# Kernel tuning notes

Measured on AMD Instinct MI355X. Metric: run time of the kernel, lower is better.

Reference implementation:

```python
import jax, jax.numpy as jnp
import numpy as np

B, T, D_IN, H, NH, R = 32, 1024, 64, 128, 4, 3
HD = H // NH  # 32


def _p(key, shape, scale=0.02):
    return jax.random.normal(key, shape, dtype=jnp.float32) * scale


def setup_inputs() -> dict:
    key = jax.random.key(0)
    ks = jax.random.split(key, 8)
    return {
        "x": jax.random.normal(ks[0], (B, T, D_IN), dtype=jnp.float32),
        "theta_w": _p(ks[1], (H, D_IN)),
        "theta_b": jnp.zeros((H,), jnp.float32),
        "in_proj_w": _p(ks[2], (3 * H, H)),
        "in_proj_b": jnp.zeros((3 * H,), jnp.float32),
        "out_proj_w": _p(ks[3], (H, H)),
        "out_proj_b": jnp.zeros((H,), jnp.float32),
        "ln_g": jnp.ones((H,), jnp.float32),
        "ln_b": jnp.zeros((H,), jnp.float32),
        "w1": _p(ks[4], (H, H)),
        "b1": jnp.zeros((H,), jnp.float32),
        "w2": _p(ks[5], (2, H)),
        "b2": jnp.zeros((2,), jnp.float32),
    }


def _build_adj(t, radius):
    # banded adjacency: adj[i,j] = 1/(1+|i-j|) for |i-j| <= radius, row-normalized
    idx = jnp.arange(t)
    d = jnp.abs(idx[:, None] - idx[None, :])
    adj = jnp.where(d <= radius, 1.0 / (1.0 + d.astype(jnp.float32)), 0.0)
    return adj / jnp.clip(adj.sum(axis=1, keepdims=True), 1e-8)


def reference(x, theta_w, theta_b, in_proj_w, in_proj_b, out_proj_w, out_proj_b,
              ln_g, ln_b, w1, b1, w2, b2):
    h = x @ theta_w.T + theta_b                       # [B,T,H]
    adj = _build_adj(T, R)                            # [T,T]
    g = jnp.einsum('ij,bjh->bih', adj, h)             # banded temporal aggregation

    # torch nn.MultiheadAttention (batch_first, eval -> no dropout)
    qkv = g @ in_proj_w.T + in_proj_b                 # [B,T,3H]
    q, k, v = jnp.split(qkv, 3, axis=-1)
    split_heads = lambda t: t.reshape(B, T, NH, HD).transpose(0, 2, 1, 3)
    q, k, v = split_heads(q), split_heads(k), split_heads(v)
    scores = jnp.einsum('bntd,bnsd->bnts', q, k) / jnp.sqrt(jnp.float32(HD))
    attn = jax.nn.softmax(scores, axis=-1)
    o = jnp.einsum('bnts,bnsd->bntd', attn, v)
    o = o.transpose(0, 2, 1, 3).reshape(B, T, H)
    a = o @ out_proj_w.T + out_proj_b                 # [B,T,H]

    # head on last timestep: LayerNorm -> Linear -> GELU(exact) -> Linear
    last = a[:, -1, :]                                # [B,H]
    mu = last.mean(-1, keepdims=True)
    var = ((last - mu) ** 2).mean(-1, keepdims=True)
    ln = (last - mu) / jnp.sqrt(var + 1e-5) * ln_g + ln_b
    hid = jax.nn.gelu(ln @ w1.T + b1, approximate=False)
    return hid @ w2.T + b2                            # [B,2]
```

## Files before the change

### kernel.cpp

```cpp
#include <hip/hip_runtime.h>
#include <math.h>

#define TT 1024

__global__ __launch_bounds__(256) void k_combine(
    const float* __restrict__ theta_w, const float* __restrict__ theta_b,
    const float* __restrict__ ipw, const float* __restrict__ ipb,
    float* __restrict__ C, float* __restrict__ bqv) {
  __shared__ float s_ipw[128 * 129];
  __shared__ float s_tw2[2][128];
  const int bidx = blockIdx.x;
  const int tid = threadIdx.x;
  if (bidx < 96) {
    const int m = bidx >> 5;
    const int dpair = bidx & 31;
    const float4* g4 = (const float4*)(ipw + m * 128 * 128);
    for (int it = 0; it < 16; ++it) {
      int idx4 = tid + it * 256;
      float4 v = g4[idx4];
      int idx = idx4 * 4;
      int e = idx >> 7;
      int c = idx & 127;
      float* dst = &s_ipw[e * 129 + c];
      dst[0] = v.x; dst[1] = v.y; dst[2] = v.z; dst[3] = v.w;
    }
    {
      int dd = tid >> 7, cc = tid & 127;
      s_tw2[dd][cc] = theta_w[cc * 64 + dpair * 2 + dd];
    }
    __syncthreads();
    const int dd = tid >> 7;
    const int e = tid & 127;
    const float* row = &s_ipw[e * 129];
    const float* tw = s_tw2[dd];
    float acc = 0.f;
    for (int c = 0; c < 128; ++c) acc += tw[c] * row[c];
    C[m * 8192 + (dpair * 2 + dd) * 128 + e] = acc;
  } else {
    const int e = tid & 127;
    const int which = tid >> 7;
    const int r0 = which ? (256 + e) : e;
    const float* row = ipw + r0 * 128;
    float acc = ipb[r0];
    for (int c = 0; c < 128; ++c) acc += theta_b[c] * row[c];
    bqv[which * 128 + e] = acc;
  }
}

__global__ __launch_bounds__(256) void k_attn(
    const float* __restrict__ x, const float* __restrict__ C,
    const float* __restrict__ bqv, float* __restrict__ o_out) {
  const int b = blockIdx.x >> 2;
  const int n = blockIdx.x & 3;
  const int tid = threadIdx.x;
  __shared__ float s_xs[64];
  __shared__ float s_q[32];
  __shared__ __align__(16) float s_r[64];
  __shared__ float s_t[TT];
  __shared__ float s_p[TT];
  __shared__ float s_pt[TT];
  __shared__ float s_red[4];
  __shared__ __align__(16) float s_uacc[4][64];
  __shared__ float s_u[64];

  const float* __restrict__ xb = x + (size_t)b * TT * 64;
  const float* Cq = C;
  const float* Ck = C + 8192;
  const float* Cv = C + 16384;

  if (tid < 64) {
    float acc = xb[(TT - 1) * 64 + tid]
              + 0.5f        * xb[(TT - 2) * 64 + tid]
              + (1.f / 3.f) * xb[(TT - 3) * 64 + tid]
              + 0.25f       * xb[(TT - 4) * 64 + tid];
    s_xs[tid] = acc * (12.f / 25.f);
  }
  __syncthreads();
  if (tid < 32) {
    float acc = bqv[n * 32 + tid];
    for (int d = 0; d < 64; ++d) acc += Cq[d * 128 + n * 32 + tid] * s_xs[d];
    s_q[tid] = acc;
  }
  __syncthreads();
  if (tid < 64) {
    float acc = 0.f;
    const float* ckr = Ck + tid * 128 + n * 32;
    for (int e = 0; e < 32; ++e) acc += ckr[e] * s_q[e];
    s_r[tid] = acc * 0.17677669529663687f;
  }
  __syncthreads();

  const int g = tid >> 4;
  const int l = tid & 15;
  const float4 r4 = ((const float4*)s_r)[l];
  for (int it = 0; it < 64; ++it) {
    const int j = it * 16 + g;
    const float4 xv = ((const float4*)(xb + j * 64))[l];
    float part = xv.x * r4.x + xv.y * r4.y + xv.z * r4.z + xv.w * r4.w;
    part += __shfl_xor(part, 1);
    part += __shfl_xor(part, 2);
    part += __shfl_xor(part, 4);
    part += __shfl_xor(part, 8);
    if (l == 0) s_t[j] = part;
  }
  __syncthreads();

  float sc[4], wsv[4];
  float lmax = -1e30f;
  const int s0 = tid * 4;
  for (int k = 0; k < 4; ++k) {
    const int s = s0 + k;
    float acc = 0.f, wsum = 0.f;
    #pragma unroll
    for (int dj = -3; dj <= 3; ++dj) {
      const int j = s + dj;
      if (j >= 0 && j < TT) {
        const float w = 1.f / (1.f + (float)(dj < 0 ? -dj : dj));
        acc += w * s_t[j];
        wsum += w;
      }
    }
    sc[k] = acc / wsum;
    wsv[k] = wsum;
    lmax = fmaxf(lmax, sc[k]);
  }
  #pragma unroll
  for (int m = 32; m >= 1; m >>= 1) lmax = fmaxf(lmax, __shfl_xor(lmax, m));
  if ((tid & 63) == 0) s_red[tid >> 6] = lmax;
  __syncthreads();
  const float bmax = fmaxf(fmaxf(s_red[0], s_red[1]), fmaxf(s_red[2], s_red[3]));
  __syncthreads();
  float lsum = 0.f;
  for (int k = 0; k < 4; ++k) {
    const float e = expf(sc[k] - bmax);
    lsum += e;
    s_p[s0 + k] = e / wsv[k];
  }
  #pragma unroll
  for (int m = 32; m >= 1; m >>= 1) lsum += __shfl_xor(lsum, m);
  if ((tid & 63) == 0) s_red[tid >> 6] = lsum;
  __syncthreads();
  const float denom = s_red[0] + s_red[1] + s_red[2] + s_red[3];
  const float inv_denom = 1.f / denom;

  for (int k = 0; k < 4; ++k) {
    const int j = s0 + k;
    float acc = 0.f;
    #pragma unroll
    for (int dj = -3; dj <= 3; ++dj) {
      const int s = j + dj;
      if (s >= 0 && s < TT)
        acc += (1.f / (1.f + (float)(dj < 0 ? -dj : dj))) * s_p[s];
    }
    s_pt[j] = acc;
  }
  __syncthreads();

  float4 u4 = make_float4(0.f, 0.f, 0.f, 0.f);
  for (int it = 0; it < 64; ++it) {
    const int j = it * 16 + g;
    const float pj = s_pt[j];
    const float4 xv = ((const float4*)(xb + j * 64))[l];
    u4.x += pj * xv.x; u4.y += pj * xv.y; u4.z += pj * xv.z; u4.w += pj * xv.w;
  }
  u4.x += __shfl_xor(u4.x, 16); u4.y += __shfl_xor(u4.y, 16);
  u4.z += __shfl_xor(u4.z, 16); u4.w += __shfl_xor(u4.w, 16);
  u4.x += __shfl_xor(u4.x, 32); u4.y += __shfl_xor(u4.y, 32);
  u4.z += __shfl_xor(u4.z, 32); u4.w += __shfl_xor(u4.w, 32);
  const int wv = tid >> 6;
  if ((tid & 63) < 16) ((float4*)s_uacc[wv])[tid & 15] = u4;
  __syncthreads();
  if (tid < 64) {
    s_u[tid] = (s_uacc[0][tid] + s_uacc[1][tid] + s_uacc[2][tid] + s_uacc[3][tid]) * inv_denom;
  }
  __syncthreads();
  if (tid < 32) {
    float acc = bqv[128 + n * 32 + tid];
    for (int d = 0; d < 64; ++d) acc += Cv[d * 128 + n * 32 + tid] * s_u[d];
    o_out[b * 128 + n * 32 + tid] = acc;
  }
}

__global__ __launch_bounds__(128) void k_epilogue(
    const float* __restrict__ o, const float* __restrict__ Wout,
    const float* __restrict__ outb, const float* __restrict__ ln_g,
    const float* __restrict__ ln_b, const float* __restrict__ w1,
    const float* __restrict__ b1, const float* __restrict__ w2,
    const float* __restrict__ b2, float* __restrict__ out) {
  const int b = blockIdx.x;
  const int e = threadIdx.x;
  __shared__ float s_o[128], s_ln[128], s_hid[128], s_red[2];
  s_o[e] = o[b * 128 + e];
  __syncthreads();
  float a = outb[e];
  {
    const float* wr = Wout + e * 128;
    for (int f = 0; f < 128; ++f) a += wr[f] * s_o[f];
  }
  float sum = a;
  #pragma unroll
  for (int m = 32; m >= 1; m >>= 1) sum += __shfl_xor(sum, m);
  if ((e & 63) == 0) s_red[e >> 6] = sum;
  __syncthreads();
  const float mu = (s_red[0] + s_red[1]) * (1.f / 128.f);
  __syncthreads();
  const float d = a - mu;
  float sq = d * d;
  #pragma unroll
  for (int m = 32; m >= 1; m >>= 1) sq += __shfl_xor(sq, m);
  if ((e & 63) == 0) s_red[e >> 6] = sq;
  __syncthreads();
  const float var = (s_red[0] + s_red[1]) * (1.f / 128.f);
  const float ln = d / sqrtf(var + 1e-5f) * ln_g[e] + ln_b[e];
  s_ln[e] = ln;
  __syncthreads();
  float h = b1[e];
  {
    const float* w1r = w1 + e * 128;
    for (int f = 0; f < 128; ++f) h += w1r[f] * s_ln[f];
  }
  h = 0.5f * h * (1.f + erff(h * 0.70710678118654752f));
  s_hid[e] = h;
  __syncthreads();
  if (e < 2) {
    float acc = b2[e];
    const float* w2r = w2 + e * 128;
    for (int f = 0; f < 128; ++f) acc += w2r[f] * s_hid[f];
    out[b * 2 + e] = acc;
  }
}

extern "C" void kernel_launch(void* const* d_in, const int* in_sizes, int n_in,
                              void* d_out, int out_size, void* d_ws, size_t ws_size,
                              hipStream_t stream) {
  const float* x       = (const float*)d_in[0];
  const float* theta_w = (const float*)d_in[1];
  const float* theta_b = (const float*)d_in[2];
  const float* ipw     = (const float*)d_in[3];
  const float* ipb     = (const float*)d_in[4];
  const float* outw    = (const float*)d_in[5];
  const float* outb    = (const float*)d_in[6];
  const float* ln_g    = (const float*)d_in[7];
  const float* ln_b    = (const float*)d_in[8];
  const float* w1      = (const float*)d_in[9];
  const float* b1      = (const float*)d_in[10];
  const float* w2      = (const float*)d_in[11];
  const float* b2      = (const float*)d_in[12];

  float* ws  = (float*)d_ws;
  float* C   = ws;
  float* bqv = ws + 24576;
  float* o   = ws + 24832;

  k_combine<<<97, 256, 0, stream>>>(theta_w, theta_b, ipw, ipb, C, bqv);
  k_attn<<<128, 256, 0, stream>>>(x, C, bqv, o);
  k_epilogue<<<32, 128, 0, stream>>>(o, outw, outb, ln_g, ln_b, w1, b1, w2, b2,
                                     (float*)d_out);
}
```

Baseline: 123.7 us.

## Split attention into chunked multi-kernel pipeline to raise parallelism over sequence

Replaces the precombined weight kernel and the per-(batch,head) attention kernel with five kernels. Per-batch query/key folding is done directly, score dot products and the probability-weighted sum over x are spread across 512 blocks covering 64-row chunks, and softmax runs separately per (batch,head). The aim is to fix low occupancy, since the old design had only 128 blocks each streaming x serially. In exchange it adds more launches and intermediate global buffers, and x is read in two separate passes.

```diff
diff --git a/kernel.cpp b/kernel.cpp
--- a/kernel.cpp
+++ b/kernel.cpp
@@ -3,70 +3,17 @@
 
 #define TT 1024
 
-__global__ __launch_bounds__(256) void k_combine(
-    const float* __restrict__ theta_w, const float* __restrict__ theta_b,
-    const float* __restrict__ ipw, const float* __restrict__ ipb,
-    float* __restrict__ C, float* __restrict__ bqv) {
-  __shared__ float s_ipw[128 * 129];
-  __shared__ float s_tw2[2][128];
-  const int bidx = blockIdx.x;
-  const int tid = threadIdx.x;
-  if (bidx < 96) {
-    const int m = bidx >> 5;
-    const int dpair = bidx & 31;
-    const float4* g4 = (const float4*)(ipw + m * 128 * 128);
-    for (int it = 0; it < 16; ++it) {
-      int idx4 = tid + it * 256;
-      float4 v = g4[idx4];
-      int idx = idx4 * 4;
-      int e = idx >> 7;
-      int c = idx & 127;
-      float* dst = &s_ipw[e * 129 + c];
-      dst[0] = v.x; dst[1] = v.y; dst[2] = v.z; dst[3] = v.w;
-    }
-    {
-      int dd = tid >> 7, cc = tid & 127;
-      s_tw2[dd][cc] = theta_w[cc * 64 + dpair * 2 + dd];
-    }
-    __syncthreads();
-    const int dd = tid >> 7;
-    const int e = tid & 127;
-    const float* row = &s_ipw[e * 129];
-    const float* tw = s_tw2[dd];
-    float acc = 0.f;
-    for (int c = 0; c < 128; ++c) acc += tw[c] * row[c];
-    C[m * 8192 + (dpair * 2 + dd) * 128 + e] = acc;
-  } else {
-    const int e = tid & 127;
-    const int which = tid >> 7;
-    const int r0 = which ? (256 + e) : e;
-    const float* row = ipw + r0 * 128;
-    float acc = ipb[r0];
-    for (int c = 0; c < 128; ++c) acc += theta_b[c] * row[c];
-    bqv[which * 128 + e] = acc;
-  }
-}
-
-__global__ __launch_bounds__(256) void k_attn(
-    const float* __restrict__ x, const float* __restrict__ C,
-    const float* __restrict__ bqv, float* __restrict__ o_out) {
-  const int b = blockIdx.x >> 2;
-  const int n = blockIdx.x & 3;
+__global__ __launch_bounds__(256) void k_qr(
+    const float* __restrict__ x, const float* __restrict__ theta_w,
+    const float* __restrict__ theta_b, const float* __restrict__ ipw,
+    const float* __restrict__ ipb, float* __restrict__ r_out) {
+  const int b = blockIdx.x;
   const int tid = threadIdx.x;
   __shared__ float s_xs[64];
-  __shared__ float s_q[32];
-  __shared__ __align__(16) float s_r[64];
-  __shared__ float s_t[TT];
-  __shared__ float s_p[TT];
-  __shared__ float s_pt[TT];
-  __shared__ float s_red[4];
-  __shared__ __align__(16) float s_uacc[4][64];
-  __shared__ float s_u[64];
-
+  __shared__ float s_y[128];
+  __shared__ float s_q[128];
+  __shared__ float s_z[4][128];
   const float* __restrict__ xb = x + (size_t)b * TT * 64;
-  const float* Cq = C;
-  const float* Ck = C + 8192;
-  const float* Cv = C + 16384;
 
   if (tid < 64) {
     float acc = xb[(TT - 1) * 64 + tid]
@@ -76,33 +23,93 @@
     s_xs[tid] = acc * (12.f / 25.f);
   }
   __syncthreads();
-  if (tid < 32) {
-    float acc = bqv[n * 32 + tid];
-    for (int d = 0; d < 64; ++d) acc += Cq[d * 128 + n * 32 + tid] * s_xs[d];
-    s_q[tid] = acc;
-  }
-  __syncthreads();
-  if (tid < 64) {
-    float acc = 0.f;
-    const float* ckr = Ck + tid * 128 + n * 32;
-    for (int e = 0; e < 32; ++e) acc += ckr[e] * s_q[e];
-    s_r[tid] = acc * 0.17677669529663687f;
-  }
-  __syncthreads();
-
-  const int g = tid >> 4;
-  const int l = tid & 15;
-  const float4 r4 = ((const float4*)s_r)[l];
-  for (int it = 0; it < 64; ++it) {
-    const int j = it * 16 + g;
-    const float4 xv = ((const float4*)(xb + j * 64))[l];
-    float part = xv.x * r4.x + xv.y * r4.y + xv.z * r4.z + xv.w * r4.w;
-    part += __shfl_xor(part, 1);
-    part += __shfl_xor(part, 2);
-    part += __shfl_xor(part, 4);
-    part += __shfl_xor(part, 8);
-    if (l == 0) s_t[j] = part;
-  }
+  if (tid < 128) {
+    const float* tr = theta_w + tid * 64;
+    float acc = theta_b[tid];
+    for (int d = 0; d < 64; ++d) acc += tr[d] * s_xs[d];
+    s_y[tid] = acc;
+  }
+  __syncthreads();
+  {
+    const int g = tid >> 4, l = tid & 15;
+    for (int pass = 0; pass < 8; ++pass) {
+      const int e = pass * 16 + g;
+      const float* wr = ipw + e * 128 + l * 8;
+      float acc = 0.f;
+      #pragma unroll
+      for (int u = 0; u < 8; ++u) acc += wr[u] * s_y[l * 8 + u];
+      acc += __shfl_xor(acc, 1);
+      acc += __shfl_xor(acc, 2);
+      acc += __shfl_xor(acc, 4);
+      acc += __shfl_xor(acc, 8);
+      if (l == 0) s_q[e] = acc + ipb[e];
+    }
+  }
+  __syncthreads();
+  for (int rep = 0; rep < 2; ++rep) {
+    const int idx = tid + rep * 256;
+    const int n = idx >> 7, c = idx & 127;
+    const float* qn = &s_q[n * 32];
+    float acc = 0.f;
+    for (int e = 0; e < 32; ++e) acc += ipw[(128 + n * 32 + e) * 128 + c] * qn[e];
+    s_z[n][c] = acc;
+  }
+  __syncthreads();
+  {
+    const int n = tid >> 6, d = tid & 63;
+    const float* zn = s_z[n];
+    float acc = 0.f;
+    for (int c = 0; c < 128; ++c) acc += theta_w[c * 64 + d] * zn[c];
+    r_out[(b * 4 + n) * 64 + d] = acc * 0.17677669529663687f;
+  }
+}
+
+__global__ __launch_bounds__(256) void k_t(
+    const float* __restrict__ x, const float* __restrict__ r_in,
+    float* __restrict__ t_out) {
+  const int b = blockIdx.x >> 4;
+  const int chunk = blockIdx.x & 15;
+  const int tid = threadIdx.x;
+  __shared__ __align__(16) float s_r[256];
+  s_r[tid] = r_in[b * 256 + tid];
+  __syncthreads();
+  const int g = tid >> 4, l = tid & 15;
+  const float4 r0 = ((const float4*)(s_r +   0))[l];
+  const float4 r1 = ((const float4*)(s_r +  64))[l];
+  const float4 r2 = ((const float4*)(s_r + 128))[l];
+  const float4 r3 = ((const float4*)(s_r + 192))[l];
+  const float* __restrict__ xb = x + ((size_t)b * TT + chunk * 64) * 64;
+  for (int it = 0; it < 4; ++it) {
+    const int jj = it * 16 + g;
+    const float4 xv = ((const float4*)(xb + jj * 64))[l];
+    float p0 = xv.x * r0.x + xv.y * r0.y + xv.z * r0.z + xv.w * r0.w;
+    float p1 = xv.x * r1.x + xv.y * r1.y + xv.z * r1.z + xv.w * r1.w;
+    float p2 = xv.x * r2.x + xv.y * r2.y + xv.z * r2.z + xv.w * r2.w;
+    float p3 = xv.x * r3.x + xv.y * r3.y + xv.z * r3.z + xv.w * r3.w;
+    #pragma unroll
+    for (int m = 1; m <= 8; m <<= 1) {
+      p0 += __shfl_xor(p0, m);
+      p1 += __shfl_xor(p1, m);
+      p2 += __shfl_xor(p2, m);
+      p3 += __shfl_xor(p3, m);
+    }
+    if (l == 0) {
+      const int j = chunk * 64 + jj;
+      t_out[(b * 4 + 0) * TT + j] = p0;
+      t_out[(b * 4 + 1) * TT + j] = p1;
+      t_out[(b * 4 + 2) * TT + j] = p2;
+      t_out[(b * 4 + 3) * TT + j] = p3;
+    }
+  }
+}
+
+__global__ __launch_bounds__(256) void k_sm(float* __restrict__ t_pt) {
+  const int bn = blockIdx.x;
+  const int tid = threadIdx.x;
+  __shared__ __align__(16) float s_t[TT];
+  __shared__ float s_p[TT];
+  __shared__ float s_red[4];
+  ((float4*)s_t)[tid] = ((const float4*)(t_pt + bn * TT))[tid];
   __syncthreads();
 
   float sc[4], wsv[4];
@@ -140,9 +147,7 @@
   for (int m = 32; m >= 1; m >>= 1) lsum += __shfl_xor(lsum, m);
   if ((tid & 63) == 0) s_red[tid >> 6] = lsum;
   __syncthreads();
-  const float denom = s_red[0] + s_red[1] + s_red[2] + s_red[3];
-  const float inv_denom = 1.f / denom;
-
+  const float inv_denom = 1.f / (s_red[0] + s_red[1] + s_red[2] + s_red[3]);
   for (int k = 0; k < 4; ++k) {
     const int j = s0 + k;
     float acc = 0.f;
@@ -152,46 +157,76 @@
       if (s >= 0 && s < TT)
         acc += (1.f / (1.f + (float)(dj < 0 ? -dj : dj))) * s_p[s];
     }
-    s_pt[j] = acc;
-  }
-  __syncthreads();
-
-  float4 u4 = make_float4(0.f, 0.f, 0.f, 0.f);
-  for (int it = 0; it < 64; ++it) {
-    const int j = it * 16 + g;
-    const float pj = s_pt[j];
-    const float4 xv = ((const float4*)(xb + j * 64))[l];
-    u4.x += pj * xv.x; u4.y += pj * xv.y; u4.z += pj * xv.z; u4.w += pj * xv.w;
-  }
-  u4.x += __shfl_xor(u4.x, 16); u4.y += __shfl_xor(u4.y, 16);
-  u4.z += __shfl_xor(u4.z, 16); u4.w += __shfl_xor(u4.w, 16);
-  u4.x += __shfl_xor(u4.x, 32); u4.y += __shfl_xor(u4.y, 32);
-  u4.z += __shfl_xor(u4.z, 32); u4.w += __shfl_xor(u4.w, 32);
-  const int wv = tid >> 6;
-  if ((tid & 63) < 16) ((float4*)s_uacc[wv])[tid & 15] = u4;
-  __syncthreads();
-  if (tid < 64) {
-    s_u[tid] = (s_uacc[0][tid] + s_uacc[1][tid] + s_uacc[2][tid] + s_uacc[3][tid]) * inv_denom;
-  }
-  __syncthreads();
-  if (tid < 32) {
-    float acc = bqv[128 + n * 32 + tid];
-    for (int d = 0; d < 64; ++d) acc += Cv[d * 128 + n * 32 + tid] * s_u[d];
-    o_out[b * 128 + n * 32 + tid] = acc;
-  }
-}
-
-__global__ __launch_bounds__(128) void k_epilogue(
-    const float* __restrict__ o, const float* __restrict__ Wout,
+    t_pt[bn * TT + j] = acc * inv_denom;
+  }
+}
+
+__global__ __launch_bounds__(256) void k_u(
+    const float* __restrict__ x, const float* __restrict__ pt_in,
+    float* __restrict__ up_out) {
+  const int b = blockIdx.x >> 4;
+  const int chunk = blockIdx.x & 15;
+  const int tid = threadIdx.x;
+  __shared__ __align__(16) float s_x[64][64];
+  __shared__ float s_p[4][64];
+  const float* __restrict__ xb = x + ((size_t)b * TT + chunk * 64) * 64;
+  #pragma unroll
+  for (int it = 0; it < 4; ++it) {
+    const int i4 = tid + it * 256;
+    ((float4*)&s_x[0][0])[i4] = ((const float4*)xb)[i4];
+  }
+  {
+    const int n = tid >> 6, jj = tid & 63;
+    s_p[n][jj] = pt_in[(b * 4 + n) * TT + chunk * 64 + jj];
+  }
+  __syncthreads();
+  const int n = tid >> 6, d = tid & 63;
+  float acc = 0.f;
+  for (int jj = 0; jj < 64; ++jj) acc += s_p[n][jj] * s_x[jj][d];
+  up_out[((b * 16 + chunk) * 4 + n) * 64 + d] = acc;
+}
+
+__global__ __launch_bounds__(128) void k_tail(
+    const float* __restrict__ up_in, const float* __restrict__ theta_w,
+    const float* __restrict__ theta_b, const float* __restrict__ ipw,
+    const float* __restrict__ ipb, const float* __restrict__ Wout,
     const float* __restrict__ outb, const float* __restrict__ ln_g,
     const float* __restrict__ ln_b, const float* __restrict__ w1,
     const float* __restrict__ b1, const float* __restrict__ w2,
     const float* __restrict__ b2, float* __restrict__ out) {
   const int b = blockIdx.x;
-  const int e = threadIdx.x;
+  const int tid = threadIdx.x;
+  __shared__ float s_u[256];
+  __shared__ float s_w[4][128];
   __shared__ float s_o[128], s_ln[128], s_hid[128], s_red[2];
-  s_o[e] = o[b * 128 + e];
-  __syncthreads();
+
+  for (int rep = 0; rep < 2; ++rep) {
+    const int idx = tid + rep * 128;
+    float acc = 0.f;
+    for (int c = 0; c < 16; ++c) acc += up_in[(b * 16 + c) * 256 + idx];
+    s_u[idx] = acc;
+  }
+  __syncthreads();
+  for (int rep = 0; rep < 4; ++rep) {
+    const int idx = tid + rep * 128;
+    const int n = idx >> 7, c = idx & 127;
+    const float* tr = theta_w + c * 64;
+    const float* un = &s_u[n * 64];
+    float acc = theta_b[c];
+    for (int d = 0; d < 64; ++d) acc += tr[d] * un[d];
+    s_w[n][c] = acc;
+  }
+  __syncthreads();
+  {
+    const int e = tid, n = e >> 5;
+    const float* wr = ipw + (256 + e) * 128;
+    const float* wn = s_w[n];
+    float acc = ipb[256 + e];
+    for (int c = 0; c < 128; ++c) acc += wr[c] * wn[c];
+    s_o[e] = acc;
+  }
+  __syncthreads();
+  const int e = tid;
   float a = outb[e];
   {
     const float* wr = Wout + e * 128;
@@ -247,13 +282,15 @@
   const float* w2      = (const float*)d_in[11];
   const float* b2      = (const float*)d_in[12];
 
-  float* ws  = (float*)d_ws;
-  float* C   = ws;
-  float* bqv = ws + 24576;
-  float* o   = ws + 24832;
-
-  k_combine<<<97, 256, 0, stream>>>(theta_w, theta_b, ipw, ipb, C, bqv);
-  k_attn<<<128, 256, 0, stream>>>(x, C, bqv, o);
-  k_epilogue<<<32, 128, 0, stream>>>(o, outw, outb, ln_g, ln_b, w1, b1, w2, b2,
-                                     (float*)d_out);
-}
+  float* ws = (float*)d_ws;
+  float* r  = ws;
+  float* t  = ws + 8192;
+  float* up = ws + 8192 + 131072;
+
+  k_qr  <<< 32, 256, 0, stream>>>(x, theta_w, theta_b, ipw, ipb, r);
+  k_t   <<<512, 256, 0, stream>>>(x, r, t);
+  k_sm  <<<128, 256, 0, stream>>>(t);
+  k_u   <<<512, 256, 0, stream>>>(x, t, up);
+  k_tail<<< 32, 128, 0, stream>>>(up, theta_w, theta_b, ipw, ipb, outw, outb,
+                                  ln_g, ln_b, w1, b1, w2, b2, (float*)d_out);
+}
```

Measured after the change: 118.0 us. 1.05x faster.
